# Performance work log

Hardware: AMD Instinct MI355X
Metric: run time of the kernel (lower is better)

Reference implementation:

```python
import jax, jax.numpy as jnp
import numpy as np

# (npoint, radius, nsample) per SA stage, from module defaults
SA_CFG = [(2048, 0.2, 64), (1024, 0.4, 32), (512, 0.6, 16), (256, 1.2, 8)]


def fps(xyz, npoint):
    """Farthest point sampling, CUDA-kernel semantics: start at index 0.
    xyz: [B,N,3] -> idx [B,npoint] int32."""
    B, N, _ = xyz.shape

    def step(carry, _):
        dist, far = carry
        centroid = jnp.take_along_axis(xyz, far[:, None, None], axis=1)  # [B,1,3]
        d = jnp.sum((xyz - centroid) ** 2, axis=-1)                      # [B,N]
        dist = jnp.minimum(dist, d)
        return (dist, jnp.argmax(dist, axis=-1).astype(jnp.int32)), far

    init = (jnp.full((B, N), 1e10, xyz.dtype), jnp.zeros((B,), jnp.int32))
    _, idxs = jax.lax.scan(step, init, None, length=npoint)  # [npoint,B]
    return idxs.T


def gather(pts, idx):
    """pts: [B,N,C], idx: [B,...] int -> [B,...,C]."""
    return jax.vmap(lambda p, i: p[i])(pts, idx)


def ball_query(xyz, new_xyz, radius, nsample):
    """First-nsample-in-ball semantics of pointnet2 ball_query; pads with the
    first found neighbor. xyz:[B,N,3], new_xyz:[B,S,3] -> [B,S,nsample] int."""
    N = xyz.shape[1]
    # squared dists via ||a||^2 + ||b||^2 - 2ab to avoid a [B,S,N,3] temp
    d2 = (jnp.sum(new_xyz ** 2, -1)[:, :, None]
          + jnp.sum(xyz ** 2, -1)[:, None, :]
          - 2.0 * jnp.einsum('bsc,bnc->bsn', new_xyz, xyz))
    cand = jnp.where(d2 < radius * radius, jnp.arange(N)[None, None, :], N)
    idx = jnp.sort(cand, axis=-1)[..., :nsample]
    first = idx[..., :1]  # center itself is always in the ball (d2==0)
    return jnp.where(idx == N, first, idx)


def sa_stage(xyz, feats, npoint, radius, nsample, layers):
    """One PointnetSAModuleVotes: FPS + ball query + normalized relative xyz
    (use_xyz=True, normalize_xyz=True) + shared MLP + max pool over nsample."""
    fidx = fps(xyz, npoint)
    new_xyz = gather(xyz, fidx)                         # [B,S,3]
    nidx = ball_query(xyz, new_xyz, radius, nsample)    # [B,S,K]
    rel = (gather(xyz, nidx) - new_xyz[:, :, None, :]) / radius  # [B,S,K,3]
    x = rel if feats is None else jnp.concatenate([rel, gather(feats, nidx)], -1)
    for w, b in layers:  # shared 1x1-conv MLP (BN folded), ReLU
        x = jax.nn.relu(x @ w + b)
    return new_xyz, jnp.max(x, axis=2)                  # [B,S,C_out]


def setup_inputs() -> dict:
    key = jax.random.key(0)
    ks = jax.random.split(key, 16)
    inp = {"pointcloud": jax.random.normal(ks[0], (4, 16384, 3), jnp.float32)}
    dims = [(3, 64, 64, 128), (131, 128, 128, 256),
            (259, 256, 256, 512), (515, 512, 512, 512)]
    k = 1
    for s, d in enumerate(dims, 1):
        for l in range(3):
            inp[f"w{s}{l}"] = jax.random.normal(
                jax.random.fold_in(ks[k], l), (d[l], d[l + 1]), jnp.float32) * 0.02
            inp[f"b{s}{l}"] = jnp.zeros((d[l + 1],), jnp.float32)
        k += 1
    return inp


def reference(pointcloud,
              w10, b10, w11, b11, w12, b12,
              w20, b20, w21, b21, w22, b22,
              w30, b30, w31, b31, w32, b32,
              w40, b40, w41, b41, w42, b42):
    stage_params = [
        [(w10, b10), (w11, b11), (w12, b12)],
        [(w20, b20), (w21, b21), (w22, b22)],
        [(w30, b30), (w31, b31), (w32, b32)],
        [(w40, b40), (w41, b41), (w42, b42)],
    ]
    xyz = pointcloud[..., :3]
    feats = None  # input_feature_dim == 0
    for (npoint, radius, nsample), layers in zip(SA_CFG, stage_params):
        xyz, feats = sa_stage(xyz, feats, npoint, radius, nsample, layers)
    return xyz, feats  # sa4_xyz [B,256,3], sa4_features [B,256,512]
```

## Files before the change

kernel.cpp:

```cpp
#include <hip/hip_runtime.h>
#include <hip/hip_bf16.h>


#define B_SZ 4

typedef float v2f __attribute__((ext_vector_type(2)));
typedef unsigned long long u64;

__device__ __forceinline__ v2f pk_add(v2f a, v2f b) {
  v2f d;
  asm("v_pk_add_f32 %0, %1, %2" : "=v"(d) : "v"(a), "v"(b));
  return d;
}
__device__ __forceinline__ v2f pk_mul(v2f a, v2f b) {
  v2f d;
  asm("v_pk_mul_f32 %0, %1, %2" : "=v"(d) : "v"(a), "v"(b));
  return d;
}

template <int CTRL>
__device__ __forceinline__ u64 dpp_u64(u64 v) {
  int lo = (int)(unsigned)v;
  int hi = (int)(unsigned)(v >> 32);
  int nlo = __builtin_amdgcn_update_dpp(lo, lo, CTRL, 0xF, 0xF, false);
  int nhi = __builtin_amdgcn_update_dpp(hi, hi, CTRL, 0xF, 0xF, false);
  return ((u64)(unsigned)nhi << 32) | (unsigned)nlo;
}

__device__ __forceinline__ u64 wave_max_u64(u64 P) {
  u64 o;
  o = dpp_u64<0x111>(P); P = o > P ? o : P;
  o = dpp_u64<0x112>(P); P = o > P ? o : P;
  o = dpp_u64<0x114>(P); P = o > P ? o : P;
  o = dpp_u64<0x118>(P); P = o > P ? o : P;
  o = dpp_u64<0x142>(P); P = o > P ? o : P;
  o = dpp_u64<0x143>(P); P = o > P ? o : P;
  return P;
}

template <int NP2>
__device__ __forceinline__ float upd_pts(const v2f* px, const v2f* py,
                                         const v2f* pz, v2f* dv, float cx,
                                         float cy, float cz) {
#pragma clang fp contract(off)
  constexpr int NACC = (NP2 >= 4) ? 4 : NP2;
  const float nx = -cx, ny = -cy, nz = -cz;
  const v2f c2x = {nx, nx}, c2y = {ny, ny}, c2z = {nz, nz};
  float mx[NACC];
#pragma unroll
  for (int q = 0; q < NACC; ++q) mx[q] = -1.0f;
#pragma unroll
  for (int j = 0; j < NP2; ++j) {
    v2f dx = pk_add(px[j], c2x);
    v2f dy = pk_add(py[j], c2y);
    v2f dz = pk_add(pz[j], c2z);
    v2f xx = pk_mul(dx, dx);
    v2f yy = pk_mul(dy, dy);
    v2f zz = pk_mul(dz, dz);
    v2f s = pk_add(xx, yy);
    v2f d = pk_add(s, zz);
    float nd0 = fminf(dv[j][0], d[0]);
    float nd1 = fminf(dv[j][1], d[1]);
    dv[j][0] = nd0; dv[j][1] = nd1;
    const int q = j % NACC;
    mx[q] = fmaxf(fmaxf(nd0, nd1), mx[q]);
  }
  float m = mx[0];
#pragma unroll
  for (int q = 1; q < NACC; ++q) m = fmaxf(m, mx[q]);
  return m;
}

template <int NP2>
__device__ __forceinline__ int rescan_idx(const v2f* dv, float m) {
  constexpr int NCH = (NP2 >= 4) ? 4 : NP2;
  constexpr int CL = NP2 / NCH;
  int bkq[NCH];
#pragma unroll
  for (int q = 0; q < NCH; ++q) {
    int bk = 0x7fffffff;
#pragma unroll
    for (int jj = CL - 1; jj >= 0; --jj) {
      int j = q * CL + jj;
      if (dv[j][1] == m) bk = 2 * j + 1;
      if (dv[j][0] == m) bk = 2 * j;
    }
    bkq[q] = bk;
  }
  int bk = bkq[NCH - 1];
#pragma unroll
  for (int q = NCH - 2; q >= 0; --q) bk = (bkq[q] != 0x7fffffff) ? bkq[q] : bk;
  return bk;
}

template <int N, int NPOINT, int T>
__global__ __launch_bounds__(T, 2) void fps1_kernel(const float* __restrict__ xyz,
                                                    int* __restrict__ fidx) {
#pragma clang fp contract(off)
  constexpr int PT = N / T;
  constexpr int NP2 = PT / 2;
  constexpr int NW = T / 64;
  const int b = blockIdx.x;
  const int t = threadIdx.x;
  const int lane = t & 63;
  const int wv = t >> 6;
  const float* base = xyz + (size_t)b * N * 3;

  v2f px[NP2], py[NP2], pz[NP2], dv[NP2];
  __shared__ __align__(16) u64 s_pack[2][NW];

#pragma unroll
  for (int j = 0; j < NP2; ++j) {
    int i0 = t + (2 * j) * T;
    int i1 = t + (2 * j + 1) * T;
    px[j][0] = base[i0 * 3 + 0]; py[j][0] = base[i0 * 3 + 1];
    pz[j][0] = base[i0 * 3 + 2];
    px[j][1] = base[i1 * 3 + 0]; py[j][1] = base[i1 * 3 + 1];
    pz[j][1] = base[i1 * 3 + 2];
    dv[j][0] = 1e10f; dv[j][1] = 1e10f;
  }

  int far = 0;
  float cenx = base[0], ceny = base[1], cenz = base[2];
  int p = 0;
  for (int it = 0; it < NPOINT; ++it) {
    if (t == 0) fidx[b * NPOINT + it] = far;
    float m = upd_pts<NP2>(px, py, pz, dv, cenx, ceny, cenz);
    int bk = rescan_idx<NP2>(dv, m);
    int idx = t + bk * T;
    u64 P = ((u64)__float_as_uint(m) << 32) | (unsigned)(N - idx);
    P = wave_max_u64(P);
    if (lane == 63) s_pack[p][wv] = P;
    __syncthreads();
    u64 bb = s_pack[p][0];
#pragma unroll
    for (int w = 1; w < NW; ++w) {
      u64 v = s_pack[p][w];
      bb = v > bb ? v : bb;
    }
    far = N - (int)(unsigned)(bb & 0xffffffffull);
    cenx = base[far * 3 + 0];
    ceny = base[far * 3 + 1];
    cenz = base[far * 3 + 2];
    p ^= 1;
  }
}

template <int N, int NPOINT>
__device__ __forceinline__ void fps_wave_body(char* smem,
                                              const float* __restrict__ xyz,
                                              int* __restrict__ fidx, int b) {
#pragma clang fp contract(off)
  constexpr int PT = N / 64;
  constexpr int NP2 = PT / 2;
  float4* s_p = (float4*)smem;
  const int lane = threadIdx.x & 63;
  const float* base = xyz + (size_t)b * N * 3;

  v2f px[NP2], py[NP2], pz[NP2], dv[NP2];
#pragma unroll
  for (int j = 0; j < NP2; ++j) {
    int i0 = lane + (2 * j) * 64;
    int i1 = lane + (2 * j + 1) * 64;
    float x0 = base[i0 * 3 + 0], y0 = base[i0 * 3 + 1], z0 = base[i0 * 3 + 2];
    float x1 = base[i1 * 3 + 0], y1 = base[i1 * 3 + 1], z1 = base[i1 * 3 + 2];
    px[j][0] = x0; py[j][0] = y0; pz[j][0] = z0;
    px[j][1] = x1; py[j][1] = y1; pz[j][1] = z1;
    dv[j][0] = 1e10f; dv[j][1] = 1e10f;
    s_p[i0] = make_float4(x0, y0, z0, 0.f);
    s_p[i1] = make_float4(x1, y1, z1, 0.f);
  }
  asm volatile("s_waitcnt lgkmcnt(0)" ::: "memory");

  int far = 0;
  float4 cen = s_p[0];
  for (int it = 0; it < NPOINT; ++it) {
    if (lane == 0) fidx[b * NPOINT + it] = far;
    float m = upd_pts<NP2>(px, py, pz, dv, cen.x, cen.y, cen.z);
    int bk = rescan_idx<NP2>(dv, m);
    int idx = lane + bk * 64;
    u64 P = ((u64)__float_as_uint(m) << 32) | (unsigned)(N - idx);
    P = wave_max_u64(P);
    far = N - __builtin_amdgcn_readlane((int)(unsigned)(P & 0xffffffffull), 63);
    cen = s_p[far];
  }
}

__global__ void gather_xyz_kernel(const float* __restrict__ xyz,
                                  const int* __restrict__ fidx,
                                  float* __restrict__ out, int N, int S) {
  int s = blockIdx.x * blockDim.x + threadIdx.x;
  int b = blockIdx.y;
  if (s < S) {
    int i = fidx[b * S + s];
    out[((size_t)(b * S + s)) * 3 + 0] = xyz[((size_t)(b * N + i)) * 3 + 0];
    out[((size_t)(b * S + s)) * 3 + 1] = xyz[((size_t)(b * N + i)) * 3 + 1];
    out[((size_t)(b * S + s)) * 3 + 2] = xyz[((size_t)(b * N + i)) * 3 + 2];
  }
}

template <int N, int NS>
__global__ __launch_bounds__(256) void ball_query_kernel(
    const float* __restrict__ xyz, const float* __restrict__ new_xyz,
    int* __restrict__ nidx, int S, float r2) {
#pragma clang fp contract(off)
  const int wv = threadIdx.x >> 6;
  const int lane = threadIdx.x & 63;
  const int b = blockIdx.y;
  const int s = blockIdx.x * 4 + wv;
  __shared__ int s_idx[4][NS];
  const float* base = xyz + (size_t)b * N * 3;

  float cx = new_xyz[((size_t)(b * S + s)) * 3 + 0];
  float cy = new_xyz[((size_t)(b * S + s)) * 3 + 1];
  float cz = new_xyz[((size_t)(b * S + s)) * 3 + 2];
  float sc = (cx * cx + cy * cy) + cz * cz;

  int found = 0;
  for (int i0 = 0; i0 < N && found < NS; i0 += 64) {
    int i = i0 + lane;
    float x = base[i * 3 + 0];
    float y = base[i * 3 + 1];
    float z = base[i * 3 + 2];
    float sx = (x * x + y * y) + z * z;
    float dt = (cx * x + cy * y) + cz * z;
    float d2 = (sc + sx) - 2.0f * dt;
    bool inb = d2 < r2;
    unsigned long long m = __ballot(inb);
    if (inb) {
      int pos = found + __popcll(m & ((1ull << lane) - 1));
      if (pos < NS) s_idx[wv][pos] = i;
    }
    found += __popcll(m);
  }
  __syncthreads();
  int fcnt = found < NS ? found : NS;
  int first = s_idx[wv][0];
  int* outp = nidx + ((size_t)(b * S + s)) * NS;
  for (int j = lane; j < NS; j += 64) outp[j] = (j < fcnt) ? s_idx[wv][j] : first;
}

template <int R, int RG, int CG, int CMAXP, int CIN, int COUT>
__device__ __forceinline__ void mlp_layer(float* act, const float* __restrict__ w,
                                          const float* __restrict__ bias, int tid) {
  constexpr int RPT = R / RG;
  constexpr int CPT = COUT / CG;
  static_assert(RG * CG == 256, "thread grid");
  const int rg = tid / CG;
  const int cg = tid % CG;

  float acc[RPT][CPT];
#pragma unroll
  for (int rr = 0; rr < RPT; ++rr)
#pragma unroll
    for (int cc = 0; cc < CPT; ++cc) acc[rr][cc] = 0.f;

  constexpr int K4 = (CIN / 4) * 4;
  for (int k = 0; k < K4; k += 4) {
    float4 a[RPT];
#pragma unroll
    for (int rr = 0; rr < RPT; ++rr)
      a[rr] = *(const float4*)(&act[(rg * RPT + rr) * CMAXP + k]);
    float wvv[4][CPT];
#pragma unroll
    for (int kk = 0; kk < 4; ++kk)
#pragma unroll
      for (int cc = 0; cc < CPT; ++cc)
        wvv[kk][cc] = w[(size_t)(k + kk) * COUT + cg + cc * CG];
#pragma unroll
    for (int rr = 0; rr < RPT; ++rr) {
      float4 av = a[rr];
#pragma unroll
      for (int cc = 0; cc < CPT; ++cc) {
        acc[rr][cc] += av.x * wvv[0][cc];
        acc[rr][cc] += av.y * wvv[1][cc];
        acc[rr][cc] += av.z * wvv[2][cc];
        acc[rr][cc] += av.w * wvv[3][cc];
      }
    }
  }
#pragma unroll 1
  for (int k = K4; k < CIN; ++k) {
    float wvv[CPT];
#pragma unroll
    for (int cc = 0; cc < CPT; ++cc) wvv[cc] = w[(size_t)k * COUT + cg + cc * CG];
#pragma unroll
    for (int rr = 0; rr < RPT; ++rr) {
      float av = act[(rg * RPT + rr) * CMAXP + k];
#pragma unroll
      for (int cc = 0; cc < CPT; ++cc) acc[rr][cc] += av * wvv[cc];
    }
  }
  __syncthreads();
#pragma unroll
  for (int rr = 0; rr < RPT; ++rr)
#pragma unroll
    for (int cc = 0; cc < CPT; ++cc) {
      int co = cg + cc * CG;
      float v = acc[rr][cc] + bias[co];
      act[(rg * RPT + rr) * CMAXP + co] = fmaxf(v, 0.f);
    }
  __syncthreads();
}

template <int NS, int G, int CPREV, int CO0, int CO1, int CO2, int RG, int CG, int CMAXP>
__device__ __forceinline__ void group_mlp_body(
    char* smem, const float* __restrict__ xyz, const float* __restrict__ new_xyz,
    const float* __restrict__ feats, const int* __restrict__ nidx,
    const float* __restrict__ w0, const float* __restrict__ b0,
    const float* __restrict__ w1, const float* __restrict__ b1,
    const float* __restrict__ w2, const float* __restrict__ b2,
    float* __restrict__ out, int N, int S, float radius, int sblk, int b) {
  constexpr int R = NS * G;
  constexpr int CIN = 3 + CPREV;
  float* act = (float*)smem;
  const int tid = threadIdx.x;
  const int s0 = sblk * G;

  for (int i = tid; i < R * CIN; i += 256) {
    int row = i / CIN;
    int ch = i - row * CIN;
    int g = row / NS;
    int j = row - g * NS;
    int sidx = s0 + g;
    int n = nidx[((size_t)(b * S + sidx)) * NS + j];
    float v;
    if constexpr (CPREV == 0) {
      v = (xyz[((size_t)(b * N + n)) * 3 + ch] -
           new_xyz[((size_t)(b * S + sidx)) * 3 + ch]) /
          radius;
    } else {
      if (ch < 3) {
        v = (xyz[((size_t)(b * N + n)) * 3 + ch] -
             new_xyz[((size_t)(b * S + sidx)) * 3 + ch]) /
            radius;
      } else {
        v = feats[((size_t)(b * N + n)) * CPREV + (ch - 3)];
      }
    }
    act[row * CMAXP + ch] = v;
  }
  __syncthreads();

  mlp_layer<R, RG, CG, CMAXP, CIN, CO0>(act, w0, b0, tid);
  mlp_layer<R, RG, CG, CMAXP, CO0, CO1>(act, w1, b1, tid);
  mlp_layer<R, RG, CG, CMAXP, CO1, CO2>(act, w2, b2, tid);

  for (int i = tid; i < G * CO2; i += 256) {
    int g = i / CO2;
    int co = i - g * CO2;
    float m = act[(g * NS) * CMAXP + co];
    for (int j = 1; j < NS; ++j) m = fmaxf(m, act[(g * NS + j) * CMAXP + co]);
    out[((size_t)(b * S + s0 + g)) * CO2 + co] = m;
  }
}

template <int NS, int G, int CPREV, int CO0, int CO1, int CO2, int RG, int CG, int CMAXP>
__global__ __launch_bounds__(256, 4) void group_mlp_kernel(
    const float* __restrict__ xyz, const float* __restrict__ new_xyz,
    const float* __restrict__ feats, const int* __restrict__ nidx,
    const float* __restrict__ w0, const float* __restrict__ b0,
    const float* __restrict__ w1, const float* __restrict__ b1,
    const float* __restrict__ w2, const float* __restrict__ b2,
    float* __restrict__ out, int N, int S, float radius) {
  __shared__ __align__(16) char smem[NS * G * CMAXP * 4];
  group_mlp_body<NS, G, CPREV, CO0, CO1, CO2, RG, CG, CMAXP>(
      smem, xyz, new_xyz, feats, nidx, w0, b0, w1, b1, w2, b2, out, N, S,
      radius, blockIdx.x, blockIdx.y);
}

template <int FN, int FNP, int NS, int G, int CPREV, int CO0, int CO1,
          int CO2, int RG, int CG, int CMAXP>
__global__ __launch_bounds__(256, 4) void fused_fps_mlp_kernel(
    const float* __restrict__ fpts, int* __restrict__ fidx,
    const float* __restrict__ xyz, const float* __restrict__ new_xyz,
    const float* __restrict__ feats, const int* __restrict__ nidx,
    const float* __restrict__ w0, const float* __restrict__ b0,
    const float* __restrict__ w1, const float* __restrict__ b1,
    const float* __restrict__ w2, const float* __restrict__ b2,
    float* __restrict__ out, int N, int S, float radius, int SBLK) {
  constexpr int FPS_B = FN * 16;
  constexpr int MLP_B = NS * G * CMAXP * 4;
  constexpr int SB = (FPS_B > MLP_B) ? FPS_B : MLP_B;
  __shared__ __align__(16) char smem[SB];
  if ((int)blockIdx.x < B_SZ) {
    if (threadIdx.x < 64) {
      __builtin_amdgcn_s_setprio(1);
      fps_wave_body<FN, FNP>(smem, fpts, fidx, blockIdx.x);
      __builtin_amdgcn_s_setprio(0);
    }
  } else {
    int bid = (int)blockIdx.x - B_SZ;
    group_mlp_body<NS, G, CPREV, CO0, CO1, CO2, RG, CG, CMAXP>(
        smem, xyz, new_xyz, feats, nidx, w0, b0, w1, b1, w2, b2, out, N, S,
        radius, bid % SBLK, bid / SBLK);
  }
}

extern "C" void kernel_launch(void* const* d_in, const int* in_sizes, int n_in,
                              void* d_out, int out_size, void* d_ws, size_t ws_size,
                              hipStream_t stream) {
  (void)in_sizes; (void)n_in; (void)out_size; (void)ws_size;
  const float* pc = (const float*)d_in[0];
  const float* W[4][3];
  const float* Bb[4][3];
  for (int s = 0; s < 4; ++s)
    for (int l = 0; l < 3; ++l) {
      W[s][l] = (const float*)d_in[1 + s * 6 + l * 2];
      Bb[s][l] = (const float*)d_in[2 + s * 6 + l * 2];
    }

  char* wsp = (char*)d_ws;
  int* fidx = (int*)wsp;
  int* nidx = (int*)(wsp + (32 << 10));
  float* xyzA = (float*)(wsp + (32 << 10) + (2 << 20));
  float* xyzB = xyzA + B_SZ * 2048 * 3;
  float* featA = xyzB + B_SZ * 2048 * 3;
  float* featB = featA + B_SZ * 2048 * 128;
  float* oxyz = (float*)d_out;
  float* ofeat = oxyz + B_SZ * 256 * 3;

  hipLaunchKernelGGL((fps1_kernel<16384, 2048, 512>), dim3(B_SZ), dim3(512), 0, stream,
                     pc, fidx);
  hipLaunchKernelGGL(gather_xyz_kernel, dim3(32, B_SZ), dim3(64), 0, stream,
                     pc, fidx, xyzA, 16384, 2048);
  hipLaunchKernelGGL((ball_query_kernel<16384, 64>), dim3(512, B_SZ), dim3(256), 0, stream,
                     pc, xyzA, nidx, 2048, (float)(0.2 * 0.2));

  hipLaunchKernelGGL((fused_fps_mlp_kernel<2048, 1024,
                                           64, 1, 0, 64, 64, 128, 8, 32, 128>),
                     dim3(B_SZ + 2048 * B_SZ), dim3(256), 0, stream,
                     xyzA, fidx,
                     pc, xyzA, (const float*)nullptr, nidx,
                     W[0][0], Bb[0][0], W[0][1], Bb[0][1], W[0][2], Bb[0][2],
                     featA, 16384, 2048, 0.2f, 2048);
  hipLaunchKernelGGL(gather_xyz_kernel, dim3(16, B_SZ), dim3(64), 0, stream,
                     xyzA, fidx, xyzB, 2048, 1024);
  hipLaunchKernelGGL((ball_query_kernel<2048, 32>), dim3(256, B_SZ), dim3(256), 0, stream,
                     xyzA, xyzB, nidx, 1024, (float)(0.4 * 0.4));

  hipLaunchKernelGGL((fused_fps_mlp_kernel<1024, 512,
                                           32, 1, 128, 128, 128, 256, 4, 64, 256>),
                     dim3(B_SZ + 1024 * B_SZ), dim3(256), 0, stream,
                     xyzB, fidx,
                     xyzA, xyzB, featA, nidx,
                     W[1][0], Bb[1][0], W[1][1], Bb[1][1], W[1][2], Bb[1][2],
                     featB, 2048, 1024, 0.4f, 1024);
  hipLaunchKernelGGL(gather_xyz_kernel, dim3(8, B_SZ), dim3(64), 0, stream,
                     xyzB, fidx, xyzA, 1024, 512);
  hipLaunchKernelGGL((ball_query_kernel<1024, 16>), dim3(128, B_SZ), dim3(256), 0, stream,
                     xyzB, xyzA, nidx, 512, (float)(0.6 * 0.6));

  hipLaunchKernelGGL((fused_fps_mlp_kernel<512, 256,
                                           16, 1, 256, 256, 256, 512, 2, 128, 512>),
                     dim3(B_SZ + 512 * B_SZ), dim3(256), 0, stream,
                     xyzA, fidx,
                     xyzB, xyzA, featB, nidx,
                     W[2][0], Bb[2][0], W[2][1], Bb[2][1], W[2][2], Bb[2][2],
                     featA, 1024, 512, 0.6f, 512);
  hipLaunchKernelGGL(gather_xyz_kernel, dim3(4, B_SZ), dim3(64), 0, stream,
                     xyzA, fidx, oxyz, 512, 256);
  hipLaunchKernelGGL((ball_query_kernel<512, 8>), dim3(64, B_SZ), dim3(256), 0, stream,
                     xyzA, oxyz, nidx, 256, (float)(1.2 * 1.2));

  hipLaunchKernelGGL((group_mlp_kernel<8, 2, 512, 512, 512, 512, 2, 128, 516>),
                     dim3(128, B_SZ), dim3(256), 0, stream,
                     xyzA, oxyz, featA, nidx,
                     W[3][0], Bb[3][0], W[3][1], Bb[3][1], W[3][2], Bb[3][2],
                     ofeat, 512, 256, 1.2f);
}
```

Baseline: 5.576 ms.

## Spread fused-stage FPS across all four waves with cross-wave LDS reduction

The FPS part of the fused FPS+MLP kernels used to run on a single wave of the 256-thread block. It now distributes the points over all 256 threads, reduces the per-wave argmax through a double-buffered LDS slot with a block barrier each iteration, and stores centroids as SoA x/y/z arrays instead of float4. This cuts the per-thread distance-update work by four but adds a __syncthreads per FPS iteration. The FPS chain is serial and sits on the critical path while the MLP blocks run alongside it.

```diff
diff --git a/kernel.cpp b/kernel.cpp
--- a/kernel.cpp
+++ b/kernel.cpp
@@ -146,43 +146,58 @@
   }
 }
 
-template <int N, int NPOINT>
-__device__ __forceinline__ void fps_wave_body(char* smem,
-                                              const float* __restrict__ xyz,
-                                              int* __restrict__ fidx, int b) {
+template <int N, int NPOINT, int T>
+__device__ __forceinline__ void fps_body_lds(char* smem,
+                                             const float* __restrict__ xyz,
+                                             int* __restrict__ fidx, int b) {
 #pragma clang fp contract(off)
-  constexpr int PT = N / 64;
+  constexpr int PT = N / T;
   constexpr int NP2 = PT / 2;
-  float4* s_p = (float4*)smem;
-  const int lane = threadIdx.x & 63;
+  constexpr int NW = T / 64;
+  u64* s_pack = (u64*)smem;
+  float* s_x = (float*)(smem + 2 * NW * sizeof(u64));
+  float* s_y = s_x + N;
+  float* s_z = s_y + N;
+  const int t = threadIdx.x;
+  const int lane = t & 63;
+  const int wv = t >> 6;
   const float* base = xyz + (size_t)b * N * 3;
 
   v2f px[NP2], py[NP2], pz[NP2], dv[NP2];
 #pragma unroll
   for (int j = 0; j < NP2; ++j) {
-    int i0 = lane + (2 * j) * 64;
-    int i1 = lane + (2 * j + 1) * 64;
-    float x0 = base[i0 * 3 + 0], y0 = base[i0 * 3 + 1], z0 = base[i0 * 3 + 2];
-    float x1 = base[i1 * 3 + 0], y1 = base[i1 * 3 + 1], z1 = base[i1 * 3 + 2];
-    px[j][0] = x0; py[j][0] = y0; pz[j][0] = z0;
-    px[j][1] = x1; py[j][1] = y1; pz[j][1] = z1;
+    int i0 = t + (2 * j) * T;
+    int i1 = t + (2 * j + 1) * T;
+    px[j][0] = base[i0 * 3 + 0]; py[j][0] = base[i0 * 3 + 1];
+    pz[j][0] = base[i0 * 3 + 2];
+    px[j][1] = base[i1 * 3 + 0]; py[j][1] = base[i1 * 3 + 1];
+    pz[j][1] = base[i1 * 3 + 2];
     dv[j][0] = 1e10f; dv[j][1] = 1e10f;
-    s_p[i0] = make_float4(x0, y0, z0, 0.f);
-    s_p[i1] = make_float4(x1, y1, z1, 0.f);
-  }
-  asm volatile("s_waitcnt lgkmcnt(0)" ::: "memory");
+    s_x[i0] = px[j][0]; s_y[i0] = py[j][0]; s_z[i0] = pz[j][0];
+    s_x[i1] = px[j][1]; s_y[i1] = py[j][1]; s_z[i1] = pz[j][1];
+  }
+  __syncthreads();
 
   int far = 0;
-  float4 cen = s_p[0];
+  int p = 0;
   for (int it = 0; it < NPOINT; ++it) {
-    if (lane == 0) fidx[b * NPOINT + it] = far;
-    float m = upd_pts<NP2>(px, py, pz, dv, cen.x, cen.y, cen.z);
+    if (t == 0) fidx[b * NPOINT + it] = far;
+    float cx = s_x[far], cy = s_y[far], cz = s_z[far];
+    float m = upd_pts<NP2>(px, py, pz, dv, cx, cy, cz);
     int bk = rescan_idx<NP2>(dv, m);
-    int idx = lane + bk * 64;
+    int idx = t + bk * T;
     u64 P = ((u64)__float_as_uint(m) << 32) | (unsigned)(N - idx);
     P = wave_max_u64(P);
-    far = N - __builtin_amdgcn_readlane((int)(unsigned)(P & 0xffffffffull), 63);
-    cen = s_p[far];
+    if (lane == 63) s_pack[p * NW + wv] = P;
+    __syncthreads();
+    u64 bbp = s_pack[p * NW + 0];
+#pragma unroll
+    for (int w = 1; w < NW; ++w) {
+      u64 v = s_pack[p * NW + w];
+      bbp = v > bbp ? v : bbp;
+    }
+    far = N - (int)(unsigned)(bbp & 0xffffffffull);
+    p ^= 1;
   }
 }
 
@@ -369,7 +384,7 @@
       radius, blockIdx.x, blockIdx.y);
 }
 
-template <int FN, int FNP, int NS, int G, int CPREV, int CO0, int CO1,
+template <int FN, int FNP, int FT, int NS, int G, int CPREV, int CO0, int CO1,
           int CO2, int RG, int CG, int CMAXP>
 __global__ __launch_bounds__(256, 4) void fused_fps_mlp_kernel(
     const float* __restrict__ fpts, int* __restrict__ fidx,
@@ -379,16 +394,14 @@
     const float* __restrict__ w1, const float* __restrict__ b1,
     const float* __restrict__ w2, const float* __restrict__ b2,
     float* __restrict__ out, int N, int S, float radius, int SBLK) {
-  constexpr int FPS_B = FN * 16;
+  constexpr int FPS_B = 2 * (FT / 64) * (int)sizeof(u64) + 3 * FN * 4;
   constexpr int MLP_B = NS * G * CMAXP * 4;
   constexpr int SB = (FPS_B > MLP_B) ? FPS_B : MLP_B;
   __shared__ __align__(16) char smem[SB];
   if ((int)blockIdx.x < B_SZ) {
-    if (threadIdx.x < 64) {
-      __builtin_amdgcn_s_setprio(1);
-      fps_wave_body<FN, FNP>(smem, fpts, fidx, blockIdx.x);
-      __builtin_amdgcn_s_setprio(0);
-    }
+    __builtin_amdgcn_s_setprio(1);
+    fps_body_lds<FN, FNP, FT>(smem, fpts, fidx, blockIdx.x);
+    __builtin_amdgcn_s_setprio(0);
   } else {
     int bid = (int)blockIdx.x - B_SZ;
     group_mlp_body<NS, G, CPREV, CO0, CO1, CO2, RG, CG, CMAXP>(
@@ -427,7 +440,7 @@
   hipLaunchKernelGGL((ball_query_kernel<16384, 64>), dim3(512, B_SZ), dim3(256), 0, stream,
                      pc, xyzA, nidx, 2048, (float)(0.2 * 0.2));
 
-  hipLaunchKernelGGL((fused_fps_mlp_kernel<2048, 1024,
+  hipLaunchKernelGGL((fused_fps_mlp_kernel<2048, 1024, 256,
                                            64, 1, 0, 64, 64, 128, 8, 32, 128>),
                      dim3(B_SZ + 2048 * B_SZ), dim3(256), 0, stream,
                      xyzA, fidx,
@@ -439,7 +452,7 @@
   hipLaunchKernelGGL((ball_query_kernel<2048, 32>), dim3(256, B_SZ), dim3(256), 0, stream,
                      xyzA, xyzB, nidx, 1024, (float)(0.4 * 0.4));
 
-  hipLaunchKernelGGL((fused_fps_mlp_kernel<1024, 512,
+  hipLaunchKernelGGL((fused_fps_mlp_kernel<1024, 512, 256,
                                            32, 1, 128, 128, 128, 256, 4, 64, 256>),
                      dim3(B_SZ + 1024 * B_SZ), dim3(256), 0, stream,
                      xyzB, fidx,
@@ -451,7 +464,7 @@
   hipLaunchKernelGGL((ball_query_kernel<1024, 16>), dim3(128, B_SZ), dim3(256), 0, stream,
                      xyzB, xyzA, nidx, 512, (float)(0.6 * 0.6));
 
-  hipLaunchKernelGGL((fused_fps_mlp_kernel<512, 256,
+  hipLaunchKernelGGL((fused_fps_mlp_kernel<512, 256, 256,
                                            16, 1, 256, 256, 256, 512, 2, 128, 512>),
                      dim3(B_SZ + 512 * B_SZ), dim3(256), 0, stream,
                      xyzA, fidx,
```

New measurement: 4.772 ms. -14.4%, faster.
